# Optimization experiments

Hardware: AMD Instinct MI355X
Metric: run time of the kernel (lower is better)

## Reference

```python
import jax, jax.numpy as jnp
import numpy as np

N = 50000   # nodes
E = 600000  # edges (avg degree ~12)
R = 8       # num_relations = 2 * n_speakers**2, n_speakers=2
B = 32      # num_bases = args.batch_size
GD, H1, H2 = 128, 128, 128


def setup_inputs() -> dict:
    key = jax.random.key(0)
    ks = jax.random.split(key, 16)
    w = lambda k, shape: jax.random.normal(k, shape, jnp.float32) * 0.05
    return {
        "node_features": jax.random.normal(ks[0], (N, GD), jnp.float32),
        "edge_index": jax.random.randint(ks[1], (2, E), 0, N),
        "edge_norm": jax.random.uniform(ks[2], (E,), jnp.float32),
        "edge_type": jax.random.randint(ks[3], (E,), 0, R),
        "basis": w(ks[4], (B, GD, H1)),
        "comp": w(ks[5], (R, B)),
        "root": w(ks[6], (GD, H1)),
        "bias1": jnp.zeros((H1,), jnp.float32),
        "w_key": w(ks[7], (H1, H2)),
        "b_key": jnp.zeros((H2,), jnp.float32),
        "w_query": w(ks[8], (H1, H2)),
        "b_query": jnp.zeros((H2,), jnp.float32),
        "w_value": w(ks[9], (H1, H2)),
        "b_value": jnp.zeros((H2,), jnp.float32),
        "w_skip": w(ks[10], (H1, H2)),
        "b_skip": jnp.zeros((H2,), jnp.float32),
    }


def reference(node_features, edge_index, edge_norm, edge_type, basis, comp,
              root, bias1, w_key, b_key, w_query, b_query, w_value, b_value,
              w_skip, b_skip):
    n = node_features.shape[0]
    r = comp.shape[0]
    src, dst = edge_index[0], edge_index[1]

    # ---- RGCNConv (basis decomposition, per-relation mean aggregation) ----
    W = jnp.einsum('rb,bio->rio', comp, basis)            # [R, GD, H1]
    xW = jnp.einsum('ni,rio->rno', node_features, W)      # [R, N, H1]
    msg = xW[edge_type, src]                              # [E, H1]
    seg = edge_type * n + dst                             # combined (relation, dst) segment id
    agg = jax.ops.segment_sum(msg, seg, num_segments=r * n).reshape(r, n, -1)
    cnt = jax.ops.segment_sum(jnp.ones(msg.shape[0], jnp.float32), seg,
                              num_segments=r * n).reshape(r, n, 1)
    h = (agg / jnp.maximum(cnt, 1.0)).sum(0) + node_features @ root + bias1

    # ---- ResGatedGraphConv: sigmoid(k_i + q_j) * v_j, sum-aggregated + skip ----
    k = h @ w_key + b_key
    q = h @ w_query + b_query
    v = h @ w_value + b_value
    m = jax.nn.sigmoid(k[dst] + q[src]) * v[src]          # [E, H2]
    out = jax.ops.segment_sum(m, dst, num_segments=n) + h @ w_skip + b_skip
    return out
```

## Files before the change

### kernel.cpp

```cpp
#include <hip/hip_runtime.h>
#include <stdint.h>

#define GD 128
#define H1 128
#define H2 128
#define NBASES 32
#define NREL 8
#define KA 1152

typedef __attribute__((ext_vector_type(8))) short bf16x8;
typedef __attribute__((ext_vector_type(4))) float f32x4;

static inline size_t align256(size_t x){ return (x + 255) & ~(size_t)255; }

__device__ __forceinline__ float bf2f(uint32_t u16){
  union { uint32_t u; float f; } c; c.u = (u16 & 0xffffu) << 16; return c.f;
}
__device__ __forceinline__ unsigned short f2bf(float f){
  union { float f; uint32_t u; } c; c.f = f;
  uint32_t u = c.u;
  u += 0x7fffu + ((u >> 16) & 1u);
  return (unsigned short)(u >> 16);
}
__device__ __forceinline__ uint32_t pkbf(float a, float b){
  union { float f; uint32_t u; } ca, cb; ca.f = a; cb.f = b;
  return __builtin_amdgcn_perm(cb.u + 0x8000u, ca.u + 0x8000u, 0x07060302u);
}
__device__ __forceinline__ float rdlanef(float v, int l){
  return __int_as_float(__builtin_amdgcn_readlane(__float_as_int(v), l));
}

__device__ __forceinline__ void async_copy16(void* lds_dst, const void* gsrc){
  __builtin_amdgcn_global_load_lds(
      (const __attribute__((address_space(1))) uint32_t*)gsrc,
      (__attribute__((address_space(3))) uint32_t*)lds_dst, 16, 0, 0);
}

__global__ void k_prep(const float* __restrict__ comp, const float* __restrict__ basis,
                       const float* __restrict__ root, unsigned short* __restrict__ Bht,
                       const float* __restrict__ wk, const float* __restrict__ wq,
                       const float* __restrict__ wv, const float* __restrict__ wsk,
                       const float* __restrict__ bk, const float* __restrict__ bq,
                       const float* __restrict__ bv, const float* __restrict__ bs,
                       unsigned short* __restrict__ B2t, float* __restrict__ Bb,
                       const float4* __restrict__ x, uint2* __restrict__ xout, int cnt4,
                       uint32_t* __restrict__ xpadz, int npadz,
                       const int* __restrict__ edst, const int* __restrict__ etyp,
                       int* __restrict__ cnt, int E, int n){
  const float LOG2E = 1.4426950408889634f;
  int b = blockIdx.x, t = threadIdx.x;
  if (b < 128){
    int i = b;
    int o = t & 127, rh = t >> 7;
    float bv[NBASES];
    #pragma unroll
    for (int bb = 0; bb < NBASES; ++bb)
      bv[bb] = basis[((size_t)bb*GD + i)*H1 + o];
    #pragma unroll
    for (int rr = 0; rr < 4; ++rr){
      int r = rh*4 + rr;
      float acc = 0.f;
      #pragma unroll
      for (int bb = 0; bb < NBASES; ++bb)
        acc += comp[r*NBASES + bb] * bv[bb];
      Bht[(size_t)o*KA + r*128 + i] = f2bf(acc);
    }
    if (rh == 1) Bht[(size_t)o*KA + 1024 + i] = f2bf(root[(size_t)i*H1 + o]);
  } else if (b < 128 + 256){
    int idx = (b - 128)*256 + t;
    int c = idx / H1, k = idx % H1;
    const float* w = (c < 128) ? wk : (c < 256) ? wq : (c < 384) ? wv : wsk;
    float val = w[(size_t)k*H2 + (c & 127)];
    if (c < 256) val *= LOG2E;
    B2t[idx] = f2bf(val);
    if (idx < 512){
      const float* bia = (idx < 128) ? bk : (idx < 256) ? bq : (idx < 384) ? bv : bs;
      float bval = bia[idx & 127];
      if (idx < 256) bval *= LOG2E;
      Bb[idx] = bval;
    }
  } else {
    int cb = b - (128 + 256);
    int ncastb = (cnt4 + 1023) >> 10;
    if (cb < ncastb){
      int base = cb*1024 + t;
      #pragma unroll
      for (int u = 0; u < 4; ++u){
        int i = base + u*256;
        if (i < cnt4){
          float4 v = x[i];
          uint2 o; o.x = pkbf(v.x, v.y); o.y = pkbf(v.z, v.w);
          xout[i] = o;
        }
      }
    } else if (cb < ncastb + 12){
      int i = (cb - ncastb)*256 + t;
      if (i < npadz) xpadz[i] = 0u;
    } else {
      int e = (cb - ncastb - 12)*256 + t;
      if (e < E) atomicAdd(&cnt[etyp[e]*n + edst[e]], 1);
    }
  }
}

__global__ void k_scanA(const int* __restrict__ deg, int* __restrict__ off,
                        int* __restrict__ btot, int len){
  __shared__ int wsum[16];
  int t = threadIdx.x, lane = t & 63, w = t >> 6;
  int i0 = blockIdx.x*8192 + t*8;
  int v[8];
  if (i0 + 7 < len){
    int4 va = *(const int4*)(deg + i0);
    int4 vb = *(const int4*)(deg + i0 + 4);
    v[0]=va.x; v[1]=va.y; v[2]=va.z; v[3]=va.w;
    v[4]=vb.x; v[5]=vb.y; v[6]=vb.z; v[7]=vb.w;
  } else {
    #pragma unroll
    for (int u = 0; u < 8; ++u) v[u] = (i0+u < len) ? deg[i0+u] : 0;
  }
  int s[8]; s[0] = v[0];
  #pragma unroll
  for (int u = 1; u < 8; ++u) s[u] = s[u-1] + v[u];
  int x = s[7];
  #pragma unroll
  for (int d = 1; d < 64; d <<= 1){
    int u = __shfl_up(x, d, 64);
    if (lane >= d) x += u;
  }
  if (lane == 63) wsum[w] = x;
  __syncthreads();
  if (t < 16){
    int y = wsum[t];
    #pragma unroll
    for (int d = 1; d < 16; d <<= 1){
      int u = __shfl_up(y, d, 16);
      if (t >= d) y += u;
    }
    wsum[t] = y;
  }
  __syncthreads();
  int woff = (w > 0) ? wsum[w-1] : 0;
  int excl = woff + x - s[7];
  #pragma unroll
  for (int u = 0; u < 8; ++u)
    if (i0+u < len) off[i0+u] = excl + s[u] - v[u];
  if (t == 0) btot[blockIdx.x] = wsum[15];
}

__global__ void k_scanB(const int* __restrict__ btot, int* __restrict__ off,
                        int* __restrict__ cursor, int len, int sentinel){
  int t = threadIdx.x, bid = blockIdx.x;
  int add = 0;
  for (int j = 0; j < bid; ++j) add += btot[j];
  int i0 = bid*8192 + t*8;
  #pragma unroll
  for (int u = 0; u < 8; ++u){
    int i = i0 + u;
    if (i < len){ int val = off[i] + add; off[i] = val; cursor[i] = val; }
  }
  if (bid == 0 && t == 0) off[len] = sentinel;
}

__global__ void k_scatter_rd(const int* __restrict__ src, const int* __restrict__ dst,
                             const int* __restrict__ typ, int* __restrict__ cursor,
                             int* __restrict__ pk, int E, int n){
  int e = blockIdx.x*blockDim.x + threadIdx.x;
  if (e >= E) return;
  int pos = atomicAdd(&cursor[typ[e]*n + dst[e]], 1);
  pk[pos] = src[e];
}

__launch_bounds__(256)
__global__ void k_fused(const int* __restrict__ off_rd, const int* __restrict__ pk_rd,
                        const uint32_t* __restrict__ x32, const unsigned short* __restrict__ xb,
                        const unsigned short* __restrict__ Bt,
                        float* __restrict__ hpart, int n, int npad){
  __shared__ char lds[49152];
  int t = threadIdx.x, lane = t & 63, wave = t >> 6;
  int row0 = blockIdx.x * 128;
  int g = blockIdx.y;
  int mrow = lane & 15, quad = lane >> 4;
  int wrow = (wave & 1) * 64, wcol = (wave >> 1) * 64;
  int s = (mrow >> 1) & 3;
  int colsw = (((t & 3) ^ ((t >> 3) & 3)) << 3);

  const unsigned short* Xsrc = xb + (size_t)(row0 + (t >> 2))*GD + colsw;
  const unsigned short* Bsrc = Bt + (size_t)(t >> 2)*KA + colsw;
  char* stage = lds + 32768;
  char* ldsw = stage + wave*1024;

  int aoff = (wrow + mrow)*64 + ((quad ^ s) << 4);
  int boff = 8192 + (wcol + mrow)*64 + ((quad ^ s) << 4);
  int axor = (mrow & 7) << 4;
  int wbase = wave*32;
  int d0 = row0 + wbase;

  f32x4 acc[4][4];
  #pragma unroll
  for (int i = 0; i < 4; ++i)
    #pragma unroll
    for (int j = 0; j < 4; ++j) acc[i][j] = (f32x4){0.f,0.f,0.f,0.f};

  for (int u = 0; u < 3; ++u){
    int r = g*3 + u;
    if (r < 8){
      __syncthreads();
      int oidx = d0 + lane; if (oidx > n) oidx = n;
      int ow = (lane < 33) ? off_rd[(size_t)r*n + oidx] : 0;
      int ownx = __shfl_down(ow, 1, 64);
      int cN = ownx - ow;
      float icN = (cN > 0) ? __builtin_amdgcn_rcpf((float)cN) : 0.f;
      int ebase = __builtin_amdgcn_readlane(ow, 0);
      int segN  = __builtin_amdgcn_readlane(ow, 32) - ebase;
      int pb[31];
      #pragma unroll
      for (int j = 0; j < 31; ++j)
        pb[j] = __builtin_amdgcn_readlane(ow, j + 1) - ebase;

      int cn = 0; float a0 = 0.f, a1 = 0.f;
#define TFLUSH(RK)                                                               \
      {                                                                          \
        float ic = rdlanef(icN, cn);                                             \
        *(uint32_t*)(lds + (wbase + cn)*256 + ((lane*4) ^ ((cn & 7) << 4)))      \
            = pkbf(a0*ic, a1*ic);                                                \
        for (int q2 = cn + 1; q2 < (RK); ++q2)                                   \
          *(uint32_t*)(lds + (wbase + q2)*256 + ((lane*4) ^ ((q2 & 7) << 4)))    \
              = 0u;                                                              \
        cn = (RK); a0 = 0.f; a1 = 0.f;                                           \
      }
      for (int jb = 0; jb < segN; jb += 64){
        int i = jb + lane;
        int node = 0;
        #pragma unroll
        for (int j = 0; j < 31; ++j) node += (i >= pb[j]);
        int m = segN - jb; if (m > 64) m = 64;
        int pj = (lane < m) ? pk_rd[ebase + i] : 0;
        int jj = 0;
        for (; jj + 8 <= m; jj += 8){
          uint32_t gg[8];
          #pragma unroll
          for (int k = 0; k < 8; ++k){
            int sN = __builtin_amdgcn_readlane(pj, jj + k);
            gg[k] = x32[(size_t)(uint32_t)sN*64 + lane];
          }
          #pragma unroll
          for (int k = 0; k < 8; ++k){
            int rk = __builtin_amdgcn_readlane(node, jj + k);
            if (rk != cn) TFLUSH(rk);
            a0 += bf2f(gg[k]); a1 += bf2f(gg[k] >> 16);
          }
        }
        for (; jj < m; jj += 4){
          int lim = m - 1;
          uint32_t gg[4];
          #pragma unroll
          for (int k = 0; k < 4; ++k){
            int tt = jj + k; if (tt > lim) tt = lim;
            int sN = __builtin_amdgcn_readlane(pj, tt);
            gg[k] = x32[(size_t)(uint32_t)sN*64 + lane];
          }
          #pragma unroll
          for (int k = 0; k < 4; ++k){
            int tt = jj + k;
            if (tt < m){
              int rk = __builtin_amdgcn_readlane(node, tt);
              if (rk != cn) TFLUSH(rk);
              a0 += bf2f(gg[k]); a1 += bf2f(gg[k] >> 16);
            }
          }
        }
      }
      TFLUSH(32)
#undef TFLUSH
      __syncthreads();
      for (int c4 = 0; c4 < 4; ++c4){
        int kts = c4*32;
        if (c4) __syncthreads();
        async_copy16(ldsw + 8192,  Bsrc + r*128 + kts);
        async_copy16(ldsw + 12288, Bsrc + (size_t)64*KA + r*128 + kts);
        __syncthreads();
        bf16x8 af[4], bf[4];
        #pragma unroll
        for (int i = 0; i < 4; ++i)
          af[i] = *(const bf16x8*)(lds + (wrow + i*16 + mrow)*256 + (((kts + quad*8)*2) ^ axor));
        #pragma unroll
        for (int j = 0; j < 4; ++j) bf[j] = *(const bf16x8*)(stage + boff + j*1024);
        #pragma unroll
        for (int i = 0; i < 4; ++i)
          #pragma unroll
          for (int j = 0; j < 4; ++j)
            acc[i][j] = __builtin_amdgcn_mfma_f32_16x16x32_bf16(af[i], bf[j], acc[i][j], 0, 0, 0);
      }
    } else {
      for (int c4 = 0; c4 < 4; ++c4){
        int kts = c4*32;
        __syncthreads();
        async_copy16(ldsw,         Xsrc + kts);
        async_copy16(ldsw + 4096,  Xsrc + (size_t)64*GD + kts);
        async_copy16(ldsw + 8192,  Bsrc + 1024 + kts);
        async_copy16(ldsw + 12288, Bsrc + (size_t)64*KA + 1024 + kts);
        __syncthreads();
        bf16x8 af[4], bf[4];
        #pragma unroll
        for (int i = 0; i < 4; ++i) af[i] = *(const bf16x8*)(stage + aoff + i*1024);
        #pragma unroll
        for (int j = 0; j < 4; ++j) bf[j] = *(const bf16x8*)(stage + boff + j*1024);
        #pragma unroll
        for (int i = 0; i < 4; ++i)
          #pragma unroll
          for (int j = 0; j < 4; ++j)
            acc[i][j] = __builtin_amdgcn_mfma_f32_16x16x32_bf16(af[i], bf[j], acc[i][j], 0, 0, 0);
      }
    }
  }
  float* hp = hpart + (size_t)g*npad*H1;
  #pragma unroll
  for (int j = 0; j < 4; ++j){
    int col = wcol + j*16 + mrow;
    #pragma unroll
    for (int i = 0; i < 4; ++i)
      #pragma unroll
      for (int rg = 0; rg < 4; ++rg){
        int row = row0 + wrow + i*16 + quad*4 + rg;
        hp[(size_t)row*H1 + col] = acc[i][j][rg];
      }
  }
}

__global__ void k_hred(const float* __restrict__ hpart, const float* __restrict__ bias1,
                       unsigned short* __restrict__ h, int npad){
  int i = blockIdx.x*blockDim.x + threadIdx.x;
  size_t stride = (size_t)npad*H1;
  float4 a = ((const float4*)hpart)[i];
  float4 b = ((const float4*)(hpart + stride))[i];
  float4 c = ((const float4*)(hpart + 2*stride))[i];
  float4 bb = ((const float4*)bias1)[i & 31];
  uint2 o;
  o.x = pkbf(a.x + b.x + c.x + bb.x, a.y + b.y + c.y + bb.y);
  o.y = pkbf(a.z + b.z + c.z + bb.z, a.w + b.w + c.w + bb.w);
  ((uint2*)h)[i] = o;
}

__launch_bounds__(256)
__global__ void k_gemm2(const unsigned short* __restrict__ A, const unsigned short* __restrict__ Bt,
                        const float* __restrict__ Bb, unsigned short* __restrict__ kqv,
                        unsigned short* __restrict__ skipb){
  __shared__ char lds[16896];
  int t = threadIdx.x, lane = t & 63, wave = t >> 6;
  int row0 = blockIdx.x * 128;
  int c0 = blockIdx.y * 128;
  int mrow = lane & 15, quad = lane >> 4;
  int wrow = (wave & 1) * 64, wcol = (wave >> 1) * 64;
  int s = (mrow >> 1) & 3;

  const unsigned short* Asrc = A + (size_t)(row0 + (t >> 2))*H1 + (((t & 3) ^ ((t >> 3) & 3)) << 3);
  const unsigned short* Bsrc = Bt + (size_t)(c0 + (t >> 2))*H1 + (((t & 3) ^ ((t >> 3) & 3)) << 3);
  char* ldsw = lds + wave*1024;

  int aoff = (wrow + mrow)*64 + ((quad ^ s) << 4);
  int boff = 8192 + (wcol + mrow)*64 + ((quad ^ s) << 4);

  f32x4 acc[4][4];
  #pragma unroll
  for (int i = 0; i < 4; ++i)
    #pragma unroll
    for (int j = 0; j < 4; ++j) acc[i][j] = (f32x4){0.f,0.f,0.f,0.f};

  #pragma unroll
  for (int kt = 0; kt < H1; kt += 32){
    __syncthreads();
    async_copy16(ldsw,         Asrc + kt);
    async_copy16(ldsw + 4096,  Asrc + (size_t)64*H1 + kt);
    async_copy16(ldsw + 8192,  Bsrc + kt);
    async_copy16(ldsw + 12288, Bsrc + (size_t)64*H1 + kt);
    __syncthreads();
    bf16x8 af[4], bf[4];
    #pragma unroll
    for (int i = 0; i < 4; ++i) af[i] = *(const bf16x8*)(lds + aoff + i*1024);
    #pragma unroll
    for (int j = 0; j < 4; ++j) bf[j] = *(const bf16x8*)(lds + boff + j*1024);
    #pragma unroll
    for (int i = 0; i < 4; ++i)
      #pragma unroll
      for (int j = 0; j < 4; ++j)
        acc[i][j] = __builtin_amdgcn_mfma_f32_16x16x32_bf16(af[i], bf[j], acc[i][j], 0, 0, 0);
  }
  float bc[4];
  #pragma unroll
  for (int j = 0; j < 4; ++j) bc[j] = Bb[c0 + wcol + j*16 + mrow];
  unsigned short* dstb; size_t ldu;
  if (c0 < 384){ dstb = kqv + c0; ldu = 384; } else { dstb = skipb; ldu = 128; }
  #pragma unroll
  for (int p = 0; p < 2; ++p){
    __syncthreads();
    if ((wave & 1) == p){
      #pragma unroll
      for (int j = 0; j < 4; ++j){
        int col = wcol + j*16 + mrow;
        #pragma unroll
        for (int i = 0; i < 4; ++i)
          #pragma unroll
          for (int rg = 0; rg < 4; ++rg){
            int rl = i*16 + quad*4 + rg;
            *(unsigned short*)(lds + rl*264 + col*2) = f2bf(acc[i][j][rg] + bc[j]);
          }
      }
    }
    __syncthreads();
    uint32_t vv[16];
    #pragma unroll
    for (int u = 0; u < 8; ++u)
      *(uint2*)&vv[u*2] = *(const uint2*)(lds + lane*264 + wave*64 + u*8);
    unsigned short* gp = dstb + (size_t)(row0 + p*64 + lane)*ldu + wave*32;
    #pragma unroll
    for (int u = 0; u < 4; ++u)
      *(uint4*)(gp + u*8) = *(const uint4*)&vv[u*4];
  }
}

__global__ void k_edge2(const int* __restrict__ off_rd, const int* __restrict__ pk_rd,
                        const unsigned short* __restrict__ kqv,
                        const unsigned short* __restrict__ skipb,
                        float* __restrict__ out, int n){
  int wid = blockIdx.x*(blockDim.x >> 6) + (threadIdx.x >> 6);
  int lane = threadIdx.x & 63;
  if (wid >= n) return;
  const uint32_t* kv32 = (const uint32_t*)kqv;
  int r = lane & 7;
  int o_r = off_rd[(size_t)r*n + wid];
  int e_r = off_rd[(size_t)r*n + wid + 1];
  int c_r = e_r - o_r;
  int c0_ = __builtin_amdgcn_readlane(c_r, 0), c1_ = __builtin_amdgcn_readlane(c_r, 1);
  int c2_ = __builtin_amdgcn_readlane(c_r, 2), c3_ = __builtin_amdgcn_readlane(c_r, 3);
  int c4_ = __builtin_amdgcn_readlane(c_r, 4), c5_ = __builtin_amdgcn_readlane(c_r, 5);
  int c6_ = __builtin_amdgcn_readlane(c_r, 6), c7_ = __builtin_amdgcn_readlane(c_r, 7);
  int o0_ = __builtin_amdgcn_readlane(o_r, 0), o1_ = __builtin_amdgcn_readlane(o_r, 1);
  int o2_ = __builtin_amdgcn_readlane(o_r, 2), o3_ = __builtin_amdgcn_readlane(o_r, 3);
  int o4_ = __builtin_amdgcn_readlane(o_r, 4), o5_ = __builtin_amdgcn_readlane(o_r, 5);
  int o6_ = __builtin_amdgcn_readlane(o_r, 6), o7_ = __builtin_amdgcn_readlane(o_r, 7);
  int p1 = c0_, p2 = p1 + c1_, p3 = p2 + c2_, p4 = p3 + c3_;
  int p5 = p4 + c4_, p6 = p5 + c5_, p7 = p6 + c6_, dg = p7 + c7_;

  uint32_t ku = kv32[(size_t)wid*192 + lane];
  float k0 = bf2f(ku), k1 = bf2f(ku >> 16);
  float a0 = 0.f, a1 = 0.f;
  for (int jb = 0; jb < dg; jb += 64){
    int i = jb + lane;
    int adj = o0_;
    adj = (i >= p1) ? (o1_ - p1) : adj;
    adj = (i >= p2) ? (o2_ - p2) : adj;
    adj = (i >= p3) ? (o3_ - p3) : adj;
    adj = (i >= p4) ? (o4_ - p4) : adj;
    adj = (i >= p5) ? (o5_ - p5) : adj;
    adj = (i >= p6) ? (o6_ - p6) : adj;
    adj = (i >= p7) ? (o7_ - p7) : adj;
    int m = dg - jb; if (m > 64) m = 64;
    int pj = (lane < m) ? pk_rd[adj + i] : 0;
    int jj = 0;
    for (; jj + 8 <= m; jj += 8){
      uint32_t qg[8], vg[8];
      #pragma unroll
      for (int k = 0; k < 8; ++k){
        int s = __builtin_amdgcn_readlane(pj, jj + k);
        const uint32_t* rowp = kv32 + (size_t)s*192 + lane;
        qg[k] = rowp[64];
        vg[k] = rowp[128];
      }
      #pragma unroll
      for (int k = 0; k < 8; ++k){
        float qq0 = bf2f(qg[k]), qq1 = bf2f(qg[k] >> 16);
        float vv0 = bf2f(vg[k]), vv1 = bf2f(vg[k] >> 16);
        float g0 = __builtin_amdgcn_rcpf(1.f + __builtin_amdgcn_exp2f(-(k0 + qq0)));
        float g1 = __builtin_amdgcn_rcpf(1.f + __builtin_amdgcn_exp2f(-(k1 + qq1)));
        a0 += g0*vv0; a1 += g1*vv1;
      }
    }
    for (; jj + 4 <= m; jj += 4){
      uint32_t qg[4], vg[4];
      #pragma unroll
      for (int k = 0; k < 4; ++k){
        int s = __builtin_amdgcn_readlane(pj, jj + k);
        const uint32_t* rowp = kv32 + (size_t)s*192 + lane;
        qg[k] = rowp[64];
        vg[k] = rowp[128];
      }
      #pragma unroll
      for (int k = 0; k < 4; ++k){
        float qq0 = bf2f(qg[k]), qq1 = bf2f(qg[k] >> 16);
        float vv0 = bf2f(vg[k]), vv1 = bf2f(vg[k] >> 16);
        float g0 = __builtin_amdgcn_rcpf(1.f + __builtin_amdgcn_exp2f(-(k0 + qq0)));
        float g1 = __builtin_amdgcn_rcpf(1.f + __builtin_amdgcn_exp2f(-(k1 + qq1)));
        a0 += g0*vv0; a1 += g1*vv1;
      }
    }
    for (; jj < m; ++jj){
      int s = __builtin_amdgcn_readlane(pj, jj);
      const uint32_t* rowp = kv32 + (size_t)s*192 + lane;
      uint32_t qg = rowp[64], vg = rowp[128];
      float qq0 = bf2f(qg), qq1 = bf2f(qg >> 16);
      float vv0 = bf2f(vg), vv1 = bf2f(vg >> 16);
      float g0 = __builtin_amdgcn_rcpf(1.f + __builtin_amdgcn_exp2f(-(k0 + qq0)));
      float g1 = __builtin_amdgcn_rcpf(1.f + __builtin_amdgcn_exp2f(-(k1 + qq1)));
      a0 += g0*vv0; a1 += g1*vv1;
    }
  }
  uint32_t sk = ((const uint32_t*)skipb)[(size_t)wid*64 + lane];
  float2 cur; cur.x = a0 + bf2f(sk); cur.y = a1 + bf2f(sk >> 16);
  ((float2*)(out + (size_t)wid*H2))[lane] = cur;
}

extern "C" void kernel_launch(void* const* d_in, const int* in_sizes, int n_in,
                              void* d_out, int out_size, void* d_ws, size_t ws_size,
                              hipStream_t stream){
  const float* x     = (const float*)d_in[0];
  const int*   eidx  = (const int*)  d_in[1];
  const int*   etype = (const int*)  d_in[3];
  const float* basis = (const float*)d_in[4];
  const float* comp  = (const float*)d_in[5];
  const float* root  = (const float*)d_in[6];
  const float* bias1 = (const float*)d_in[7];
  const float* wk    = (const float*)d_in[8];
  const float* bk    = (const float*)d_in[9];
  const float* wq    = (const float*)d_in[10];
  const float* bq    = (const float*)d_in[11];
  const float* wv    = (const float*)d_in[12];
  const float* bv    = (const float*)d_in[13];
  const float* wsk   = (const float*)d_in[14];
  const float* bs    = (const float*)d_in[15];
  const int n = in_sizes[0] / GD;
  const int E = in_sizes[3];
  const int npad = (n + 127) & ~127;
  const int* esrc = eidx;
  const int* edst = eidx + E;
  float* out = (float*)d_out;

  char* w = (char*)d_ws;
  size_t off = 0;
  unsigned short* xbf  = (unsigned short*)(w + off); off = align256(off + (size_t)npad*GD*2);
  unsigned short* Bht  = (unsigned short*)(w + off); off = align256(off + (size_t)KA*H1*2);
  unsigned short* B2t  = (unsigned short*)(w + off); off = align256(off + (size_t)512*H1*2);
  float* Bb            = (float*)(w + off);          off = align256(off + 512*4);
  unsigned short* hbuf = (unsigned short*)(w + off); off = align256(off + (size_t)npad*H1*2);
  float* hpart         = (float*)(w + off);          off = align256(off + (size_t)3*npad*H1*4);
  unsigned short* kqv  = (unsigned short*)(w + off); off = align256(off + (size_t)npad*384*2);
  unsigned short* skipb= (unsigned short*)(w + off); off = align256(off + (size_t)npad*H2*2);
  int* cnt_rd          = (int*)(w + off);            off = align256(off + (size_t)(8*n+4)*4);
  int* off_rd          = (int*)(w + off);            off = align256(off + (size_t)(8*n+1)*4);
  int* cur_rd          = (int*)(w + off);            off = align256(off + (size_t)8*n*4);
  int* btot_rd         = (int*)(w + off);            off = align256(off + 64*4);
  int* pk_rd           = (int*)(w + off);            off = align256(off + (size_t)E*4);

  const int nblk_rd = (8*n + 8191) / 8192;
  const int cnt4 = n*GD/4;
  const int ncastb = (cnt4 + 1023)/1024;
  const int histb  = (E + 255)/256;
  const int npadz  = (npad - n)*GD/2;

  hipMemsetAsync(cnt_rd, 0, (size_t)8*n*4, stream);

  k_prep<<<128 + 256 + ncastb + 12 + histb, 256, 0, stream>>>(
      comp, basis, root, Bht, wk, wq, wv, wsk, bk, bq, bv, bs, B2t, Bb,
      (const float4*)x, (uint2*)xbf, cnt4,
      (uint32_t*)(xbf + (size_t)n*GD), npadz,
      edst, etype, cnt_rd, E, n);
  k_scanA<<<nblk_rd, 1024, 0, stream>>>(cnt_rd, off_rd, btot_rd, 8*n);
  k_scanB<<<nblk_rd, 1024, 0, stream>>>(btot_rd, off_rd, cur_rd, 8*n, E);
  k_scatter_rd<<<(E + 255)/256, 256, 0, stream>>>(esrc, edst, etype, cur_rd, pk_rd, E, n);
  k_fused<<<dim3(npad/128, 3), 256, 0, stream>>>(off_rd, pk_rd, (const uint32_t*)xbf, xbf,
                                                 Bht, hpart, n, npad);
  k_hred<<<npad*H1/4/256, 256, 0, stream>>>(hpart, bias1, hbuf, npad);
  k_gemm2<<<dim3(npad/128, 4), 256, 0, stream>>>(hbuf, B2t, Bb, kqv, skipb);
  k_edge2<<<(n + 3)/4, 256, 0, stream>>>(off_rd, pk_rd, kqv, skipb, out, n);
}
```

Measured before the change: 348.2 us.

## Double-buffer relation gather in fused RGCN kernel with smaller row tiles

The fused aggregation+GEMM kernel now processes 64 destination rows per block instead of 128, doubling the grid. It double-buffers the gathered per-relation tile in LDS so the next relation's gather runs before the current relation's MFMA pass, with one barrier per step. B and X operands are now read directly from global memory into registers instead of being staged through LDS with async copies. The aim is fewer barriers, lower LDS use and overlap of gather latency with compute, at the cost of uncoalesced or repeated global reads of the weight matrix and less reuse per block.

```diff
diff --git a/kernel.cpp b/kernel.cpp
--- a/kernel.cpp
+++ b/kernel.cpp
@@ -175,150 +175,147 @@
                         const uint32_t* __restrict__ x32, const unsigned short* __restrict__ xb,
                         const unsigned short* __restrict__ Bt,
                         float* __restrict__ hpart, int n, int npad){
-  __shared__ char lds[49152];
+  __shared__ char lds[32768];
   int t = threadIdx.x, lane = t & 63, wave = t >> 6;
-  int row0 = blockIdx.x * 128;
+  int row0 = blockIdx.x * 64;
   int g = blockIdx.y;
   int mrow = lane & 15, quad = lane >> 4;
-  int wrow = (wave & 1) * 64, wcol = (wave >> 1) * 64;
-  int s = (mrow >> 1) & 3;
-  int colsw = (((t & 3) ^ ((t >> 3) & 3)) << 3);
-
-  const unsigned short* Xsrc = xb + (size_t)(row0 + (t >> 2))*GD + colsw;
-  const unsigned short* Bsrc = Bt + (size_t)(t >> 2)*KA + colsw;
-  char* stage = lds + 32768;
-  char* ldsw = stage + wave*1024;
-
-  int aoff = (wrow + mrow)*64 + ((quad ^ s) << 4);
-  int boff = 8192 + (wcol + mrow)*64 + ((quad ^ s) << 4);
+  int wrow = (wave & 1) * 32, wcol = (wave >> 1) * 64;
   int axor = (mrow & 7) << 4;
-  int wbase = wave*32;
+  int wbase = wave*16;
   int d0 = row0 + wbase;
 
-  f32x4 acc[4][4];
-  #pragma unroll
-  for (int i = 0; i < 4; ++i)
+  const unsigned short* Bp = Bt + (size_t)(wcol + mrow)*KA + quad*8;
+
+  f32x4 acc[2][4];
+  #pragma unroll
+  for (int i = 0; i < 2; ++i)
     #pragma unroll
     for (int j = 0; j < 4; ++j) acc[i][j] = (f32x4){0.f,0.f,0.f,0.f};
 
+#define TFLUSH(RK, TB)                                                           \
+      {                                                                          \
+        float ic = rdlanef(icN, cn);                                             \
+        *(uint32_t*)((TB) + (wbase + cn)*256 + ((lane*4) ^ ((cn & 7) << 4)))     \
+            = pkbf(a0*ic, a1*ic);                                                \
+        for (int q2 = cn + 1; q2 < (RK); ++q2)                                   \
+          *(uint32_t*)((TB) + (wbase + q2)*256 + ((lane*4) ^ ((q2 & 7) << 4)))   \
+              = 0u;                                                              \
+        cn = (RK); a0 = 0.f; a1 = 0.f;                                           \
+      }
+
+#define GATHER(RR, TB)                                                           \
+  {                                                                              \
+    int oidx = d0 + lane; if (oidx > n) oidx = n;                                \
+    int ow = (lane < 17) ? off_rd[(size_t)(RR)*n + oidx] : 0;                    \
+    int ownx = __shfl_down(ow, 1, 64);                                           \
+    int cN = ownx - ow;                                    \
+    float icN = (cN > 0) ? __builtin_amdgcn_rcpf((float)cN) : 0.f;               \
+    int ebase = __builtin_amdgcn_readlane(ow, 0);                                \
+    int segN  = __builtin_amdgcn_readlane(ow, 16) - ebase;                       \
+    int cn = 0; float a0 = 0.f, a1 = 0.f;                                        \
+    for (int jb = 0; jb < segN; jb += 64){                                       \
+      int i = jb + lane;                                                         \
+      int node = 0;                                                              \
+      _Pragma("unroll")                                                          \
+      for (int j = 0; j < 15; ++j)                                               \
+        node += (i >= (__builtin_amdgcn_readlane(ow, j + 1) - ebase));           \
+      int m = segN - jb; if (m > 64) m = 64;                                     \
+      int pj = (lane < m) ? pk_rd[ebase + i] : 0;                                \
+      int jj = 0;                                                                \
+      for (; jj + 8 <= m; jj += 8){                                              \
+        uint32_t gg[8];                                                          \
+        _Pragma("unroll")                                                        \
+        for (int k = 0; k < 8; ++k){                                             \
+          int sN = __builtin_amdgcn_readlane(pj, jj + k);                        \
+          gg[k] = x32[(size_t)(uint32_t)sN*64 + lane];                           \
+        }                                                                        \
+        _Pragma("unroll")                                                        \
+        for (int k = 0; k < 8; ++k){                                             \
+          int rk = __builtin_amdgcn_readlane(node, jj + k);                      \
+          if (rk != cn) TFLUSH(rk, TB);                                          \
+          a0 += bf2f(gg[k]); a1 += bf2f(gg[k] >> 16);                            \
+        }                                                                        \
+      }                                                                          \
+      for (; jj < m; jj += 4){                          \
+        int lim = m - 1;                                                         \
+        uint32_t gg[4];                                                          \
+        _Pragma("unroll")                                                        \
+        for (int k = 0; k < 4; ++k){                                             \
+          int tt = jj + k; if (tt > lim) tt = lim;                               \
+          int sN = __builtin_amdgcn_readlane(pj, tt);                            \
+          gg[k] = x32[(size_t)(uint32_t)sN*64 + lane];                           \
+        }                                                                        \
+        _Pragma("unroll")                                                        \
+        for (int k = 0; k < 4; ++k){                                             \
+          int tt = jj + k;                                                       \
+          if (tt < m){                                                           \
+            int rk = __builtin_amdgcn_readlane(node, tt);                        \
+            if (rk != cn) TFLUSH(rk, TB);                                        \
+            a0 += bf2f(gg[k]); a1 += bf2f(gg[k] >> 16);                          \
+          }                                                                      \
+        }                                                                        \
+      }                                                                          \
+    }                                                                            \
+    TFLUSH(16, TB)                                                               \
+  }
+
+  GATHER(g*3, lds)
+  __syncthreads();
+  int cur = 0;
   for (int u = 0; u < 3; ++u){
     int r = g*3 + u;
+    if (u < 2){
+      int rn = r + 1;
+      if (rn < 8) GATHER(rn, lds + (cur^1)*16384)
+    }
     if (r < 8){
-      __syncthreads();
-      int oidx = d0 + lane; if (oidx > n) oidx = n;
-      int ow = (lane < 33) ? off_rd[(size_t)r*n + oidx] : 0;
-      int ownx = __shfl_down(ow, 1, 64);
-      int cN = ownx - ow;
-      float icN = (cN > 0) ? __builtin_amdgcn_rcpf((float)cN) : 0.f;
-      int ebase = __builtin_amdgcn_readlane(ow, 0);
-      int segN  = __builtin_amdgcn_readlane(ow, 32) - ebase;
-      int pb[31];
-      #pragma unroll
-      for (int j = 0; j < 31; ++j)
-        pb[j] = __builtin_amdgcn_readlane(ow, j + 1) - ebase;
-
-      int cn = 0; float a0 = 0.f, a1 = 0.f;
-#define TFLUSH(RK)                                                               \
-      {                                                                          \
-        float ic = rdlanef(icN, cn);                                             \
-        *(uint32_t*)(lds + (wbase + cn)*256 + ((lane*4) ^ ((cn & 7) << 4)))      \
-            = pkbf(a0*ic, a1*ic);                                                \
-        for (int q2 = cn + 1; q2 < (RK); ++q2)                                   \
-          *(uint32_t*)(lds + (wbase + q2)*256 + ((lane*4) ^ ((q2 & 7) << 4)))    \
-              = 0u;                                                              \
-        cn = (RK); a0 = 0.f; a1 = 0.f;                                           \
-      }
-      for (int jb = 0; jb < segN; jb += 64){
-        int i = jb + lane;
-        int node = 0;
-        #pragma unroll
-        for (int j = 0; j < 31; ++j) node += (i >= pb[j]);
-        int m = segN - jb; if (m > 64) m = 64;
-        int pj = (lane < m) ? pk_rd[ebase + i] : 0;
-        int jj = 0;
-        for (; jj + 8 <= m; jj += 8){
-          uint32_t gg[8];
-          #pragma unroll
-          for (int k = 0; k < 8; ++k){
-            int sN = __builtin_amdgcn_readlane(pj, jj + k);
-            gg[k] = x32[(size_t)(uint32_t)sN*64 + lane];
-          }
-          #pragma unroll
-          for (int k = 0; k < 8; ++k){
-            int rk = __builtin_amdgcn_readlane(node, jj + k);
-            if (rk != cn) TFLUSH(rk);
-            a0 += bf2f(gg[k]); a1 += bf2f(gg[k] >> 16);
-          }
-        }
-        for (; jj < m; jj += 4){
-          int lim = m - 1;
-          uint32_t gg[4];
-          #pragma unroll
-          for (int k = 0; k < 4; ++k){
-            int tt = jj + k; if (tt > lim) tt = lim;
-            int sN = __builtin_amdgcn_readlane(pj, tt);
-            gg[k] = x32[(size_t)(uint32_t)sN*64 + lane];
-          }
-          #pragma unroll
-          for (int k = 0; k < 4; ++k){
-            int tt = jj + k;
-            if (tt < m){
-              int rk = __builtin_amdgcn_readlane(node, tt);
-              if (rk != cn) TFLUSH(rk);
-              a0 += bf2f(gg[k]); a1 += bf2f(gg[k] >> 16);
-            }
-          }
-        }
-      }
-      TFLUSH(32)
-#undef TFLUSH
-      __syncthreads();
+      const char* tb = lds + cur*16384;
+      #pragma unroll
       for (int c4 = 0; c4 < 4; ++c4){
         int kts = c4*32;
-        if (c4) __syncthreads();
-        async_copy16(ldsw + 8192,  Bsrc + r*128 + kts);
-        async_copy16(ldsw + 12288, Bsrc + (size_t)64*KA + r*128 + kts);
-        __syncthreads();
-        bf16x8 af[4], bf[4];
-        #pragma unroll
-        for (int i = 0; i < 4; ++i)
-          af[i] = *(const bf16x8*)(lds + (wrow + i*16 + mrow)*256 + (((kts + quad*8)*2) ^ axor));
-        #pragma unroll
-        for (int j = 0; j < 4; ++j) bf[j] = *(const bf16x8*)(stage + boff + j*1024);
-        #pragma unroll
-        for (int i = 0; i < 4; ++i)
+        bf16x8 af[2], bf[4];
+        #pragma unroll
+        for (int i = 0; i < 2; ++i)
+          af[i] = *(const bf16x8*)(tb + (wrow + i*16 + mrow)*256 + (((kts + quad*8)*2) ^ axor));
+        #pragma unroll
+        for (int j = 0; j < 4; ++j)
+          bf[j] = *(const bf16x8*)(Bp + (size_t)j*16*KA + r*128 + kts);
+        #pragma unroll
+        for (int i = 0; i < 2; ++i)
           #pragma unroll
           for (int j = 0; j < 4; ++j)
             acc[i][j] = __builtin_amdgcn_mfma_f32_16x16x32_bf16(af[i], bf[j], acc[i][j], 0, 0, 0);
       }
     } else {
+      #pragma unroll
       for (int c4 = 0; c4 < 4; ++c4){
         int kts = c4*32;
-        __syncthreads();
-        async_copy16(ldsw,         Xsrc + kts);
-        async_copy16(ldsw + 4096,  Xsrc + (size_t)64*GD + kts);
-        async_copy16(ldsw + 8192,  Bsrc + 1024 + kts);
-        async_copy16(ldsw + 12288, Bsrc + (size_t)64*KA + 1024 + kts);
-        __syncthreads();
-        bf16x8 af[4], bf[4];
-        #pragma unroll
-        for (int i = 0; i < 4; ++i) af[i] = *(const bf16x8*)(stage + aoff + i*1024);
-        #pragma unroll
-        for (int j = 0; j < 4; ++j) bf[j] = *(const bf16x8*)(stage + boff + j*1024);
-        #pragma unroll
-        for (int i = 0; i < 4; ++i)
+        bf16x8 af[2], bf[4];
+        #pragma unroll
+        for (int i = 0; i < 2; ++i)
+          af[i] = *(const bf16x8*)(xb + (size_t)(row0 + wrow + i*16 + mrow)*GD + kts + quad*8);
+        #pragma unroll
+        for (int j = 0; j < 4; ++j)
+          bf[j] = *(const bf16x8*)(Bp + (size_t)j*16*KA + 1024 + kts);
+        #pragma unroll
+        for (int i = 0; i < 2; ++i)
           #pragma unroll
           for (int j = 0; j < 4; ++j)
             acc[i][j] = __builtin_amdgcn_mfma_f32_16x16x32_bf16(af[i], bf[j], acc[i][j], 0, 0, 0);
       }
     }
-  }
+    __syncthreads();
+    cur ^= 1;
+  }
+#undef GATHER
+#undef TFLUSH
   float* hp = hpart + (size_t)g*npad*H1;
   #pragma unroll
   for (int j = 0; j < 4; ++j){
     int col = wcol + j*16 + mrow;
     #pragma unroll
-    for (int i = 0; i < 4; ++i)
+    for (int i = 0; i < 2; ++i)
       #pragma unroll
       for (int rg = 0; rg < 4; ++rg){
         int row = row0 + wrow + i*16 + quad*4 + rg;
@@ -566,8 +563,8 @@
   k_scanA<<<nblk_rd, 1024, 0, stream>>>(cnt_rd, off_rd, btot_rd, 8*n);
   k_scanB<<<nblk_rd, 1024, 0, stream>>>(btot_rd, off_rd, cur_rd, 8*n, E);
   k_scatter_rd<<<(E + 255)/256, 256, 0, stream>>>(esrc, edst, etype, cur_rd, pk_rd, E, n);
-  k_fused<<<dim3(npad/128, 3), 256, 0, stream>>>(off_rd, pk_rd, (const uint32_t*)xbf, xbf,
-                                                 Bht, hpart, n, npad);
+  k_fused<<<dim3(npad/64, 3), 256, 0, stream>>>(off_rd, pk_rd, (const uint32_t*)xbf, xbf,
+                                                Bht, hpart, n, npad);
   k_hred<<<npad*H1/4/256, 256, 0, stream>>>(hpart, bias1, hbuf, npad);
   k_gemm2<<<dim3(npad/128, 4), 256, 0, stream>>>(hbuf, B2t, Bb, kqv, skipb);
   k_edge2<<<(n + 3)/4, 256, 0, stream>>>(off_rd, pk_rd, kqv, skipb, out, n);
```

Result: slower. 385.2 us (+10.6%).
